# Kernel tuning notes

Hardware: AMD Instinct MI355X
Metric: run time of the kernel (lower is better)

## Reference

```python
import jax, jax.numpy as jnp
import numpy as np

N_BLOCKS = 32   # n complex Jordan blocks (2x2 each)
M_REAL = 64     # m real eigenvalues
DT = 0.01       # time step
BATCH = 131072
DIM = 2 * N_BLOCKS + M_REAL  # 128


def setup_inputs() -> dict:
    key = jax.random.key(0)
    k1, k2 = jax.random.split(key)
    x = jax.random.normal(k1, (BATCH, DIM), dtype=jnp.float32)
    Lambda = jax.random.normal(k2, (BATCH, DIM), dtype=jnp.float32)
    return {"x": x, "Lambda": Lambda}


def reference(x, Lambda):
    # Block-diagonal Koopman advance: A is block-diag of n 2x2 rotation-scalings
    # (exp(mu*dt)*[[cos, -sin],[sin, cos]]) and m scalar exp(lambda*dt) entries.
    # We apply it directly to x without materializing A (same math as A @ x).
    n, m, dt = N_BLOCKS, M_REAL, DT
    mu = Lambda[:, :n]            # [B, n]
    omega = Lambda[:, n:2 * n]    # [B, n]
    lam = Lambda[:, 2 * n:]       # [B, m]

    e = jnp.exp(mu * dt)          # [B, n]
    c = jnp.cos(omega * dt)
    s = jnp.sin(omega * dt)

    xc = x[:, :2 * n].reshape(-1, n, 2)  # [B, n, 2] (even, odd) components
    x0, x1 = xc[..., 0], xc[..., 1]
    y0 = e * (c * x0 - s * x1)    # row [exp*cos, -exp*sin]
    y1 = e * (s * x0 + c * x1)    # row [exp*sin,  exp*cos]
    yc = jnp.stack([y0, y1], axis=-1).reshape(-1, 2 * n)  # [B, 2n]

    yr = jnp.exp(lam * dt) * x[:, 2 * n:]  # [B, m]
    return jnp.concatenate([yc, yr], axis=-1)  # [B, d]
```

## Files before the change

kernel.cpp:

```cpp
#include <hip/hip_runtime.h>

#define BATCH   131072
#define NB      32
#define DIM     128
#define DT      0.01f
#define VEC_PER_ROW (DIM / 4)

__global__ __launch_bounds__(256) void
koopman_kernel(const float4* __restrict__ x4,
               const float*  __restrict__ L,
               float4* __restrict__ out4)
{
    int t = blockIdx.x * blockDim.x + threadIdx.x;
    int row = t >> 5;
    int j   = t & 31;

    float4 xv = x4[t];
    const float* Lr = L + (size_t)row * DIM;
    float4 o;

    if (j < 16) {
        float2 mu = *(const float2*)(Lr + 2 * j);
        float2 om = *(const float2*)(Lr + NB + 2 * j);

        float e0 = __expf(mu.x * DT);
        float e1 = __expf(mu.y * DT);
        float s0, c0, s1, c1;
        __sincosf(om.x * DT, &s0, &c0);
        __sincosf(om.y * DT, &s1, &c1);

        o.x = e0 * (c0 * xv.x - s0 * xv.y);
        o.y = e0 * (s0 * xv.x + c0 * xv.y);
        o.z = e1 * (c1 * xv.z - s1 * xv.w);
        o.w = e1 * (s1 * xv.z + c1 * xv.w);
    } else {
        float4 lam = *(const float4*)(Lr + 4 * j);
        o.x = __expf(lam.x * DT) * xv.x;
        o.y = __expf(lam.y * DT) * xv.y;
        o.z = __expf(lam.z * DT) * xv.z;
        o.w = __expf(lam.w * DT) * xv.w;
    }

    out4[t] = o;
}

extern "C" void kernel_launch(void* const* d_in, const int* in_sizes, int n_in,
                              void* d_out, int out_size, void* d_ws, size_t ws_size,
                              hipStream_t stream)
{
    const float4* x4 = (const float4*)d_in[0];
    const float*  L  = (const float*)d_in[1];
    float4* out4     = (float4*)d_out;

    const int total_vec = BATCH * VEC_PER_ROW;
    const int block = 256;
    const int grid  = total_vec / block;

    koopman_kernel<<<grid, block, 0, stream>>>(x4, L, out4);
}
```

Before: 165.5 us.

## Process rows with eight threads each, removing branch divergence and widening loads

Reassigns work so each thread handles four float4 chunks of a row: two complex-block chunks and two real-eigenvalue chunks. Every thread now runs the same code path, which removes the divergence between the complex and real halves inside a wavefront. Lambda is loaded as float4 instead of float2. Per-thread accesses become strided pairs, which may reduce coalescing efficiency per instruction, and the grid is four times smaller.

```diff
diff --git a/kernel.cpp b/kernel.cpp
--- a/kernel.cpp
+++ b/kernel.cpp
@@ -4,44 +4,59 @@
 #define NB      32
 #define DIM     128
 #define DT      0.01f
-#define VEC_PER_ROW (DIM / 4)
+#define THREADS_PER_ROW 8
 
 __global__ __launch_bounds__(256) void
 koopman_kernel(const float4* __restrict__ x4,
-               const float*  __restrict__ L,
+               const float4* __restrict__ L4,
                float4* __restrict__ out4)
 {
-    int t = blockIdx.x * blockDim.x + threadIdx.x;
-    int row = t >> 5;
-    int j   = t & 31;
+    int t   = blockIdx.x * blockDim.x + threadIdx.x;
+    int row = t >> 3;
+    int j   = t & 7;
+    int base = row * (DIM / 4);
 
-    float4 xv = x4[t];
-    const float* Lr = L + (size_t)row * DIM;
-    float4 o;
+    float4 xa  = x4[base + 2 * j];
+    float4 xb  = x4[base + 2 * j + 1];
+    float4 mu  = L4[base + j];
+    float4 om  = L4[base + 8 + j];
+    float4 xr0 = x4[base + 16 + 2 * j];
+    float4 xr1 = x4[base + 17 + 2 * j];
+    float4 l0  = L4[base + 16 + 2 * j];
+    float4 l1  = L4[base + 17 + 2 * j];
 
-    if (j < 16) {
-        float2 mu = *(const float2*)(Lr + 2 * j);
-        float2 om = *(const float2*)(Lr + NB + 2 * j);
+    float e0 = __expf(mu.x * DT), e1 = __expf(mu.y * DT);
+    float e2 = __expf(mu.z * DT), e3 = __expf(mu.w * DT);
+    float s0, c0, s1, c1, s2, c2, s3, c3;
+    __sincosf(om.x * DT, &s0, &c0);
+    __sincosf(om.y * DT, &s1, &c1);
+    __sincosf(om.z * DT, &s2, &c2);
+    __sincosf(om.w * DT, &s3, &c3);
 
-        float e0 = __expf(mu.x * DT);
-        float e1 = __expf(mu.y * DT);
-        float s0, c0, s1, c1;
-        __sincosf(om.x * DT, &s0, &c0);
-        __sincosf(om.y * DT, &s1, &c1);
+    float4 oa, ob;
+    oa.x = e0 * (c0 * xa.x - s0 * xa.y);
+    oa.y = e0 * (s0 * xa.x + c0 * xa.y);
+    oa.z = e1 * (c1 * xa.z - s1 * xa.w);
+    oa.w = e1 * (s1 * xa.z + c1 * xa.w);
+    ob.x = e2 * (c2 * xb.x - s2 * xb.y);
+    ob.y = e2 * (s2 * xb.x + c2 * xb.y);
+    ob.z = e3 * (c3 * xb.z - s3 * xb.w);
+    ob.w = e3 * (s3 * xb.z + c3 * xb.w);
 
-        o.x = e0 * (c0 * xv.x - s0 * xv.y);
-        o.y = e0 * (s0 * xv.x + c0 * xv.y);
-        o.z = e1 * (c1 * xv.z - s1 * xv.w);
-        o.w = e1 * (s1 * xv.z + c1 * xv.w);
-    } else {
-        float4 lam = *(const float4*)(Lr + 4 * j);
-        o.x = __expf(lam.x * DT) * xv.x;
-        o.y = __expf(lam.y * DT) * xv.y;
-        o.z = __expf(lam.z * DT) * xv.z;
-        o.w = __expf(lam.w * DT) * xv.w;
-    }
+    float4 or0, or1;
+    or0.x = __expf(l0.x * DT) * xr0.x;
+    or0.y = __expf(l0.y * DT) * xr0.y;
+    or0.z = __expf(l0.z * DT) * xr0.z;
+    or0.w = __expf(l0.w * DT) * xr0.w;
+    or1.x = __expf(l1.x * DT) * xr1.x;
+    or1.y = __expf(l1.y * DT) * xr1.y;
+    or1.z = __expf(l1.z * DT) * xr1.z;
+    or1.w = __expf(l1.w * DT) * xr1.w;
 
-    out4[t] = o;
+    out4[base + 2 * j]      = oa;
+    out4[base + 2 * j + 1]  = ob;
+    out4[base + 16 + 2 * j] = or0;
+    out4[base + 17 + 2 * j] = or1;
 }
 
 extern "C" void kernel_launch(void* const* d_in, const int* in_sizes, int n_in,
@@ -49,12 +64,12 @@
                               hipStream_t stream)
 {
     const float4* x4 = (const float4*)d_in[0];
-    const float*  L  = (const float*)d_in[1];
+    const float4* L4 = (const float4*)d_in[1];
     float4* out4     = (float4*)d_out;
 
-    const int total_vec = BATCH * VEC_PER_ROW;
+    const int total_threads = BATCH * THREADS_PER_ROW;
     const int block = 256;
-    const int grid  = total_vec / block;
+    const int grid  = total_threads / block;
 
-    koopman_kernel<<<grid, block, 0, stream>>>(x4, L, out4);
+    koopman_kernel<<<grid, block, 0, stream>>>(x4, L4, out4);
 }
```

New measurement: 167.7 us. Within noise of the previous version (+1.3%).
